# Optimization experiments

Hardware: AMD Instinct MI355X
Metric: run time of the kernel (lower is better)

## Reference

```python
import jax, jax.numpy as jnp
import numpy as np

B, C1, C2, N1, N2 = 8, 16, 32, 256, 128


def _masks():
    # static numpy masks, mirroring EquivariantLayer.__init__
    n_max, n_min = max(N1, N2), min(N1, N2)
    k = np.arange(n_max)
    k[k > n_max // 2] -= n_max
    mask = np.abs(k) <= n_min / 2            # |k| <= n_min/2 (both nyquists)
    mask2 = mask[: n_max // 2 + 1].copy()    # taken BEFORE removing neg nyquist
    nyq_pos = k == n_min / 2
    nyq_pos2 = nyq_pos[: n_max // 2 + 1]
    nyq_neg = k == -n_min / 2
    mask[nyq_neg] = False                    # drop negative nyquist row
    return mask, mask2, nyq_pos, nyq_pos2

MASK, MASK2, NYQ_POS, NYQ_POS2 = _masks()


def rot90_kernel(t):
    # 90-deg rotation about grid point [0,0] for periodic kernels:
    # transpose last two dims, keep column 0, reverse remaining columns
    t = jnp.swapaxes(t, -1, -2)
    return jnp.concatenate([t[..., :1], t[..., 1:][..., ::-1]], axis=-1)


def symmetric_kernel(kernel):
    # average over the 8 elements of D4 (rotations + transpose*rotations)
    k1 = kernel
    k2 = rot90_kernel(k1)
    k3 = rot90_kernel(k2)
    k4 = rot90_kernel(k3)
    k5 = jnp.swapaxes(k1, -1, -2)
    k6 = rot90_kernel(k5)
    k7 = rot90_kernel(k6)
    k8 = rot90_kernel(k7)
    return (k1 + k2 + k3 + k4 + k5 + k6 + k7 + k8) / 8.0


def _forward(f, kernel):
    F = jnp.fft.rfft2(f)                                  # [b,c1,N1,N1//2+1]
    # downsample: zero nyquist modes, truncate spectrum, rescale
    F = jnp.where(jnp.asarray(NYQ_POS)[None, None, :, None], 0, F)
    F = jnp.where(jnp.asarray(NYQ_POS2)[None, None, None, :], 0, F)
    F = F[:, :, MASK, :][:, :, :, MASK2] * (N2 / N1) ** 2  # [b,c1,N2,N2//2+1]
    # spectral convolution with D4-symmetrized kernel
    K = jnp.fft.rfft2(symmetric_kernel(kernel))            # [1,c1,c2,N2,N2//2+1]
    conv = jnp.einsum('bcnk,cdnk->bdnk', F, K[0])          # sum over input channels
    return jnp.fft.irfft2(F), jnp.fft.irfft2(conv)


def setup_inputs() -> dict:
    key = jax.random.key(0)
    kf, kk = jax.random.split(key)
    f = jax.random.normal(kf, (B, C1, N1, N1), dtype=jnp.float32)
    eps = 0.1
    kernel = eps * (2.0 * jax.random.uniform(kk, (1, C1, C2, N2, N2), dtype=jnp.float32) - 1.0)
    return {"f": f, "kernel": kernel}


def reference(f, kernel):
    return _forward(f, kernel)
```

## Files before the change

### kernel.cpp

```cpp
#include <hip/hip_runtime.h>

#define PI_F 3.14159265358979f

typedef unsigned int  uint32;
typedef unsigned short ushort16;

__device__ __forceinline__ float2 cmul(float2 a, float2 b) {
    return make_float2(a.x * b.x - a.y * b.y, a.x * b.y + a.y * b.x);
}
__device__ __forceinline__ float2 cadd(float2 a, float2 b) { return make_float2(a.x + b.x, a.y + b.y); }
__device__ __forceinline__ float2 csub(float2 a, float2 b) { return make_float2(a.x - b.x, a.y - b.y); }
__device__ __forceinline__ float2 shflx(float2 v, int m) {
    return make_float2(__shfl_xor(v.x, m, 64), __shfl_xor(v.y, m, 64));
}
__device__ __forceinline__ float2 shfli(float2 v, int src) {
    return make_float2(__shfl(v.x, src, 64), __shfl(v.y, src, 64));
}
__device__ __forceinline__ int brev6(int x) { return (int)(__brev((unsigned)x) >> 26); }

__device__ __forceinline__ uint32 bfu(float x) {
    uint32 u = __float_as_uint(x);
    return (u + 0x7FFFu + ((u >> 16) & 1u)) >> 16;
}
__device__ __forceinline__ uint32 packbf2(float2 v) { return bfu(v.x) | (bfu(v.y) << 16); }
__device__ __forceinline__ float2 unpackbf2(uint32 u) {
    return make_float2(__uint_as_float(u << 16), __uint_as_float(u & 0xFFFF0000u));
}
__device__ __forceinline__ float bf2f(ushort16 u) { return __uint_as_float((uint32)u << 16); }

template<int CTRL>
__device__ __forceinline__ float dpp1(float x) {
    return __builtin_bit_cast(float, __builtin_amdgcn_update_dpp(
        0, __builtin_bit_cast(int, x), CTRL, 0xF, 0xF, true));
}
template<int CTRL>
__device__ __forceinline__ float2 dppx(float2 v) {
    return make_float2(dpp1<CTRL>(v.x), dpp1<CTRL>(v.y));
}

__device__ __forceinline__ float swz4(float x) {
    return __int_as_float(__builtin_amdgcn_ds_swizzle(__float_as_int(x), 0x101F));
}

template<bool INV>
__device__ __forceinline__ void tw_init(int lane, float2* w, float* sg) {
#pragma unroll
    for (int t = 0; t < 6; ++t) {
        int m = 32 >> t;
        bool up = (lane & m) != 0;
        int pos = lane & (m - 1);
        float ang = (INV ? PI_F : -PI_F) * (float)pos / (float)m;
        float sn, cs;
        __sincosf(ang, &sn, &cs);
        w[t]  = up ? make_float2(cs, sn) : make_float2(1.f, 0.f);
        sg[t] = (t < 2) ? (up ? -2.f : 0.f) : (up ? -1.f : 1.f);
    }
}

__device__ __forceinline__ float2 fft64s(float2 v, const float2* w, const float* sg) {
#if __has_builtin(__builtin_amdgcn_permlane32_swap) && __has_builtin(__builtin_amdgcn_permlane16_swap)
    {
        auto rx = __builtin_amdgcn_permlane32_swap(__float_as_uint(v.x), __float_as_uint(v.x), false, false);
        auto ry = __builtin_amdgcn_permlane32_swap(__float_as_uint(v.y), __float_as_uint(v.y), false, false);
        float2 d = make_float2(
            fmaf(sg[0], v.x, __uint_as_float(rx[0]) + __uint_as_float(rx[1])),
            fmaf(sg[0], v.y, __uint_as_float(ry[0]) + __uint_as_float(ry[1])));
        v = cmul(d, w[0]);
    }
    {
        auto rx = __builtin_amdgcn_permlane16_swap(__float_as_uint(v.x), __float_as_uint(v.x), false, false);
        auto ry = __builtin_amdgcn_permlane16_swap(__float_as_uint(v.y), __float_as_uint(v.y), false, false);
        float2 d = make_float2(
            fmaf(sg[1], v.x, __uint_as_float(rx[0]) + __uint_as_float(rx[1])),
            fmaf(sg[1], v.y, __uint_as_float(ry[0]) + __uint_as_float(ry[1])));
        v = cmul(d, w[1]);
    }
#else
    {   float2 p = shflx(v, 32); float s0 = 1.0f + sg[0];
        float2 d = make_float2(fmaf(s0, v.x, p.x), fmaf(s0, v.y, p.y));
        v = cmul(d, w[0]);
    }
    {   float2 p = shflx(v, 16); float s1 = 1.0f + sg[1];
        float2 d = make_float2(fmaf(s1, v.x, p.x), fmaf(s1, v.y, p.y));
        v = cmul(d, w[1]);
    }
#endif
    {
        float2 p = dppx<0x128>(v);
        float2 d = make_float2(fmaf(sg[2], v.x, p.x), fmaf(sg[2], v.y, p.y));
        v = cmul(d, w[2]);
    }
    {
        float2 p = make_float2(swz4(v.x), swz4(v.y));
        float2 d = make_float2(fmaf(sg[3], v.x, p.x), fmaf(sg[3], v.y, p.y));
        v = cmul(d, w[3]);
    }
    {
        float2 p = dppx<0x4E>(v);
        float2 d = make_float2(fmaf(sg[4], v.x, p.x), fmaf(sg[4], v.y, p.y));
        v = cmul(d, w[4]);
    }
    {
        float2 p = dppx<0xB1>(v);
        float2 d = make_float2(fmaf(sg[5], v.x, p.x), fmaf(sg[5], v.y, p.y));
        v = cmul(d, w[5]);
    }
    return v;
}

__device__ __forceinline__ int s66(int r, int c) {
    return r * 66 + (c ^ (((r >> 4) & 3) << 4));
}

__device__ void kfft_body(const float* __restrict__ kin, ushort16* __restrict__ kout,
                          float2* X, int img) {
    int lane = threadIdx.x & 63, wv = threadIdx.x >> 6;
    float2 w[6]; float sg[6];
    tw_init<false>(lane, w, sg);
    int b6 = brev6(lane);
    float sn, cs;
    __sincosf(-PI_F * (float)lane * (1.0f / 64.0f), &sn, &cs);
    float2 w64 = make_float2(cs, sn);
    __sincosf(-PI_F * (float)b6 * (1.0f / 64.0f), &sn, &cs);
    float2 wub = make_float2(cs, sn);
    const float2* in2 = (const float2*)(kin + (size_t)img * 16384);
    int gm2 = brev6((64 - b6) & 63);
#pragma unroll 2
    for (int rr = 0; rr < 16; ++rr) {
        int r = wv * 16 + rr;
        float2 z = in2[r * 64 + lane];
        z = fft64s(z, w, sg);
        float2 zm = shfli(z, gm2);
        float ar = z.x + zm.x, ai = z.y - zm.y;
        float br = z.x - zm.x, bi = z.y + zm.y;
        float p = wub.x * br - wub.y * bi, q = wub.x * bi + wub.y * br;
        X[r * 65 + b6] = make_float2(0.5f * (ar + q), 0.5f * (ai - p));
    }
    __syncthreads();
    float2 c0[8], c1[8];
#pragma unroll
    for (int cc = 0; cc < 8; ++cc) {
        int k = wv * 8 + cc;
        c0[cc] = X[lane * 65 + k];
        c1[cc] = X[(lane + 64) * 65 + k];
    }
    __syncthreads();
    float* Rr = (float*)X;
#pragma unroll
    for (int cc = 0; cc < 8; ++cc) {
        int k = wv * 8 + cc;
        float2 r0 = c0[cc], r1 = c1[cc];
        float2 t = r0;
        r0 = cadd(t, r1);
        r1 = cmul(csub(t, r1), w64);
        r0 = fft64s(r0, w, sg);
        r1 = fft64s(r1, w, sg);
        Rr[(2 * b6) * 65 + k]     = r0.x;
        Rr[(2 * b6 + 1) * 65 + k] = r1.x;
    }
    __syncthreads();
    ushort4* ko4 = (ushort4*)(kout + (size_t)img * 8192);
    for (int i = threadIdx.x; i < 2048; i += 512) {
        int n = i >> 4, k4 = (i & 15) << 2;
        float op[4];
#pragma unroll
        for (int m = 0; m < 4; ++m) {
            int k = k4 + m;
            float t1 = Rr[n * 65 + k];
            float t2 = Rr[((128 - n) & 127) * 65 + k];
            float t3, t4;
            if (n < 64) {
                t3 = Rr[k * 65 + n];
                t4 = Rr[((128 - k) & 127) * 65 + n];
            } else {
                int c2 = 128 - n; if (c2 > 63) c2 = 63;
                t3 = Rr[((128 - k) & 127) * 65 + c2];
                t4 = Rr[k * 65 + c2];
            }
            op[m] = 0.25f * (t1 + t2 + t3 + t4);
        }
        ushort4 o4;
        o4.x = (ushort16)bfu(op[0]); o4.y = (ushort16)bfu(op[1]);
        o4.z = (ushort16)bfu(op[2]); o4.w = (ushort16)bfu(op[3]);
        ko4[i] = o4;
    }
}

__device__ void ffull_body(const float* __restrict__ f, uint32* __restrict__ FH,
                           uint32* S, int img) {
    int lane = threadIdx.x & 63, wv = threadIdx.x >> 6;
    float2 w[6]; float sg[6];
    tw_init<false>(lane, w, sg);
    float sn, cs;
    __sincosf(-PI_F * (float)lane * (1.0f / 64.0f), &sn, &cs);
    float2 w64 = make_float2(cs, sn);
    int m = brev6(lane);
    __sincosf(-PI_F * (float)(2 * m) * (1.0f / 128.0f), &sn, &cs);
    float2 wue = make_float2(cs, sn);
    __sincosf(-PI_F * (float)(2 * m + 1) * (1.0f / 128.0f), &sn, &cs);
    float2 wuo = make_float2(cs, sn);
    int src_e = brev6((64 - m) & 63);
    int src_o = brev6(63 - m);
    bool active = (lane & 1) == 0;
    const float* fimg = f + (size_t)img * 65536;
#pragma unroll 2
    for (int rr = 0; rr < 32; ++rr) {
        int r = wv * 32 + rr;
        const float2* x = (const float2*)(fimg + r * 256);
        float2 r0 = x[lane], r1 = x[lane + 64];
        float2 t = r0;
        r0 = cadd(t, r1);
        r1 = cmul(csub(t, r1), w64);
        r0 = fft64s(r0, w, sg);
        r1 = fft64s(r1, w, sg);
        float2 zme = shfli(r0, src_e);
        float2 zmo = shfli(r1, src_o);
        float ar = r0.x + zme.x, ai = r0.y - zme.y;
        float br = r0.x - zme.x, bi = r0.y + zme.y;
        float p = wue.x * br - wue.y * bi, q = wue.x * bi + wue.y * br;
        uint32 xe = packbf2(make_float2(0.5f * (ar + q), 0.5f * (ai - p)));
        ar = r1.x + zmo.x; ai = r1.y - zmo.y;
        br = r1.x - zmo.x; bi = r1.y + zmo.y;
        p = wuo.x * br - wuo.y * bi; q = wuo.x * bi + wuo.y * br;
        uint32 xo = packbf2(make_float2(0.5f * (ar + q), 0.5f * (ai - p)));
        if (active) *(uint2*)&S[s66(r, 2 * m)] = make_uint2(xe, xo);
    }
    __syncthreads();
    __sincosf(-PI_F * (float)lane * (1.0f / 128.0f), &sn, &cs);
    float2 w128a = make_float2(cs, sn);
    __sincosf(-PI_F * (float)(lane + 64) * (1.0f / 128.0f), &sn, &cs);
    float2 w128b = make_float2(cs, sn);
    int b6 = brev6(lane);
#pragma unroll
    for (int ch = 0; ch < 4; ++ch) {
        float2 q0[2], q1[2], q2[2], q3[2];
#pragma unroll
        for (int cc = 0; cc < 2; ++cc) {
            int c = wv * 8 + ch * 2 + cc;
            q0[cc] = unpackbf2(S[s66(lane,       c)]);
            q1[cc] = unpackbf2(S[s66(lane +  64, c)]);
            q2[cc] = unpackbf2(S[s66(lane + 128, c)]);
            q3[cc] = unpackbf2(S[s66(lane + 192, c)]);
        }
#pragma unroll
        for (int cc = 0; cc < 2; ++cc) {
            int c = wv * 8 + ch * 2 + cc;
            float2 r0 = q0[cc], r1 = q1[cc], r2 = q2[cc], r3 = q3[cc], t;
            t = r0; r0 = cadd(t, r2); r2 = cmul(csub(t, r2), w128a);
            t = r1; r1 = cadd(t, r3); r3 = cmul(csub(t, r3), w128b);
            t = r0; r0 = cadd(t, r1); r1 = cmul(csub(t, r1), w64);
            t = r2; r2 = cadd(t, r3); r3 = cmul(csub(t, r3), w64);
            r0 = fft64s(r0, w, sg); r1 = fft64s(r1, w, sg);
            r2 = fft64s(r2, w, sg); r3 = fft64s(r3, w, sg);
            float2 vv[4] = { r0, r2, r1, r3 };
#pragma unroll
            for (int j = 0; j < 4; ++j) {
                int n = 4 * b6 + j;
                int r = (n < 64) ? n : ((n >= 193) ? n - 128 : -1);
                if (r >= 0)
                    S[s66(r, c)] = packbf2(make_float2(vv[j].x * 0.25f, vv[j].y * 0.25f));
            }
        }
    }
    __syncthreads();
    uint32* dst = FH + (size_t)img * 8192;
    for (int i = threadIdx.x; i < 8192; i += 512) {
        int r = i >> 6, c = i & 63;
        dst[i] = (r == 64) ? 0u : S[s66(r, c)];
    }
}

__global__ __launch_bounds__(512) void mega_a(const float* __restrict__ kin,
                                              ushort16* __restrict__ Kr,
                                              const float* __restrict__ f,
                                              uint32* __restrict__ FH) {
    __shared__ uint32 SH[256 * 66];
    int bid = blockIdx.x;
    if (bid < 128) ffull_body(f, FH, SH, bid);
    else           kfft_body(kin, Kr, (float2*)SH, bid - 128);
}

__device__ void einsum_body(const uint32* __restrict__ F, const ushort16* __restrict__ K,
                            uint32* __restrict__ C, uint32* Ft, int bid) {
    int nk0 = bid * 32;
    int t = threadIdx.x;
    for (int i = t; i < 4096; i += 512) {
        int bc = i >> 5, nl = i & 31;
        Ft[i] = F[(size_t)bc * 8192 + nk0 + nl];
    }
    __syncthreads();
    int nl = t & 31, dg = t >> 5;
    int nk = nk0 + nl;
    float2 acc[2][8] = {};
#pragma unroll
    for (int c = 0; c < 16; ++c) {
        float2 fv[8];
#pragma unroll
        for (int b = 0; b < 8; ++b) fv[b] = unpackbf2(Ft[(b * 16 + c) * 32 + nl]);
#pragma unroll
        for (int j = 0; j < 2; ++j) {
            int d = j * 16 + dg;
            float kv = bf2f(K[(size_t)(c * 32 + d) * 8192 + nk]);
#pragma unroll
            for (int b = 0; b < 8; ++b) {
                acc[j][b].x = fmaf(fv[b].x, kv, acc[j][b].x);
                acc[j][b].y = fmaf(fv[b].y, kv, acc[j][b].y);
            }
        }
    }
#pragma unroll
    for (int j = 0; j < 2; ++j) {
        int d = j * 16 + dg;
#pragma unroll
        for (int b = 0; b < 8; ++b)
            C[(size_t)(b * 32 + d) * 8192 + nk] = packbf2(acc[j][b]);
    }
}

__device__ void ifuse_body(const uint32* __restrict__ src, float2* __restrict__ dst,
                           float2* S) {
    int lane = threadIdx.x & 63, wv = threadIdx.x >> 6;
    float2 w[6]; float sg[6];
    tw_init<true>(lane, w, sg);
    float sn, cs;
    __sincosf(PI_F * (float)lane * (1.0f / 64.0f), &sn, &cs);
    float2 w64 = make_float2(cs, sn);
    for (int i = threadIdx.x; i < 8192; i += 512) {
        int r = i >> 6, c = i & 63;
        S[r * 65 + c] = unpackbf2(src[i]);
    }
    __syncthreads();
    int b6 = brev6(lane);
#pragma unroll
    for (int cc = 0; cc < 8; ++cc) {
        int k = wv * 8 + cc;
        float2 r0 = S[lane * 65 + k];
        float2 r1 = S[(lane + 64) * 65 + k];
        float2 t = r0;
        r0 = cadd(t, r1);
        r1 = cmul(csub(t, r1), w64);
        r0 = fft64s(r0, w, sg);
        r1 = fft64s(r1, w, sg);
        S[(2 * b6) * 65 + k]     = r0;
        S[(2 * b6 + 1) * 65 + k] = r1;
    }
    __syncthreads();
#pragma unroll 2
    for (int rr = 0; rr < 16; ++rr) {
        int m = wv * 16 + rr;
        float2 X = S[m * 65 + lane];
        float2 Xm = shfli(X, (64 - lane) & 63);
        if (lane == 0) Xm = make_float2(0.f, 0.f);
        float er = 0.5f * (X.x + Xm.x), ei = 0.5f * (X.y - Xm.y);
        float br = 0.5f * (X.x - Xm.x), bi = 0.5f * (X.y + Xm.y);
        float orr = w64.x * br - w64.y * bi, oi = w64.x * bi + w64.y * br;
        float2 Z = make_float2(er - oi, ei + orr);
        Z = fft64s(Z, w, sg);
        dst[m * 64 + b6] = make_float2(Z.x * (1.0f / 8192.0f), Z.y * (1.0f / 8192.0f));
    }
}

__global__ __launch_bounds__(512) void mega2(const uint32* __restrict__ FH,
                                             const ushort16* __restrict__ Kr,
                                             uint32* __restrict__ CONV,
                                             float* __restrict__ out) {
    __shared__ float2 SH[128 * 65];
    int bid = blockIdx.x;
    if (bid < 256) einsum_body(FH, Kr, CONV, (uint32*)SH, bid);
    else {
        int img = bid - 256;
        ifuse_body(FH + (size_t)img * 8192, (float2*)(out + (size_t)img * 16384), SH);
    }
}

__global__ __launch_bounds__(512) void ifuse1(const uint32* __restrict__ CV,
                                              float* __restrict__ out1) {
    __shared__ float2 SH[128 * 65];
    int img = blockIdx.x;
    ifuse_body(CV + (size_t)img * 8192, (float2*)(out1 + (size_t)img * 16384), SH);
}

extern "C" void kernel_launch(void* const* d_in, const int* in_sizes, int n_in,
                              void* d_out, int out_size, void* d_ws, size_t ws_size,
                              hipStream_t stream) {
    const float* f   = (const float*)d_in[0];
    const float* kin = (const float*)d_in[1];
    float* out = (float*)d_out;
    char* ws = (char*)d_ws;

    uint32*   CONV = (uint32*)ws;
    uint32*   FHAT = (uint32*)(ws + 8388608);
    ushort16* Kr   = (ushort16*)(ws + 16777216);

    mega_a<<<640, 512, 0, stream>>>(kin, Kr, f, FHAT);
    mega2<<<384, 512, 0, stream>>>(FHAT, Kr, CONV, out);
    ifuse1<<<256, 512, 0, stream>>>(CONV, out + 2097152);
}
```

Before: 161.5 us.

## Fuse channel-contraction einsum into the inverse FFT blocks, dropping CONV buffer

Each inverse-FFT block for the conv output now computes its own (b,d) spectrum by contracting over the 16 input channels directly into shared memory, then runs the inverse FFT. This removes the separate einsum pass, the bf16 CONV round-trip through global memory, and one kernel launch. In exchange the F spectra are re-read once per output channel (32x redundancy, though likely L2-resident) and the K reads lose the batch reuse the old einsum had.

```diff
diff --git a/kernel.cpp b/kernel.cpp
--- a/kernel.cpp
+++ b/kernel.cpp
@@ -280,56 +280,13 @@
     else           kfft_body(kin, Kr, (float2*)SH, bid - 128);
 }
 
-__device__ void einsum_body(const uint32* __restrict__ F, const ushort16* __restrict__ K,
-                            uint32* __restrict__ C, uint32* Ft, int bid) {
-    int nk0 = bid * 32;
-    int t = threadIdx.x;
-    for (int i = t; i < 4096; i += 512) {
-        int bc = i >> 5, nl = i & 31;
-        Ft[i] = F[(size_t)bc * 8192 + nk0 + nl];
-    }
-    __syncthreads();
-    int nl = t & 31, dg = t >> 5;
-    int nk = nk0 + nl;
-    float2 acc[2][8] = {};
-#pragma unroll
-    for (int c = 0; c < 16; ++c) {
-        float2 fv[8];
-#pragma unroll
-        for (int b = 0; b < 8; ++b) fv[b] = unpackbf2(Ft[(b * 16 + c) * 32 + nl]);
-#pragma unroll
-        for (int j = 0; j < 2; ++j) {
-            int d = j * 16 + dg;
-            float kv = bf2f(K[(size_t)(c * 32 + d) * 8192 + nk]);
-#pragma unroll
-            for (int b = 0; b < 8; ++b) {
-                acc[j][b].x = fmaf(fv[b].x, kv, acc[j][b].x);
-                acc[j][b].y = fmaf(fv[b].y, kv, acc[j][b].y);
-            }
-        }
-    }
-#pragma unroll
-    for (int j = 0; j < 2; ++j) {
-        int d = j * 16 + dg;
-#pragma unroll
-        for (int b = 0; b < 8; ++b)
-            C[(size_t)(b * 32 + d) * 8192 + nk] = packbf2(acc[j][b]);
-    }
-}
-
-__device__ void ifuse_body(const uint32* __restrict__ src, float2* __restrict__ dst,
-                           float2* S) {
+__device__ void ifuse_core(float2* S, float2* __restrict__ dst) {
     int lane = threadIdx.x & 63, wv = threadIdx.x >> 6;
     float2 w[6]; float sg[6];
     tw_init<true>(lane, w, sg);
     float sn, cs;
     __sincosf(PI_F * (float)lane * (1.0f / 64.0f), &sn, &cs);
     float2 w64 = make_float2(cs, sn);
-    for (int i = threadIdx.x; i < 8192; i += 512) {
-        int r = i >> 6, c = i & 63;
-        S[r * 65 + c] = unpackbf2(src[i]);
-    }
-    __syncthreads();
     int b6 = brev6(lane);
 #pragma unroll
     for (int cc = 0; cc < 8; ++cc) {
@@ -360,24 +317,55 @@
     }
 }
 
-__global__ __launch_bounds__(512) void mega2(const uint32* __restrict__ FH,
-                                             const ushort16* __restrict__ Kr,
-                                             uint32* __restrict__ CONV,
-                                             float* __restrict__ out) {
+__device__ void ifuse_body(const uint32* __restrict__ src, float2* __restrict__ dst,
+                           float2* S) {
+    for (int i = threadIdx.x; i < 8192; i += 512) {
+        int r = i >> 6, c = i & 63;
+        S[r * 65 + c] = unpackbf2(src[i]);
+    }
+    __syncthreads();
+    ifuse_core(S, dst);
+}
+
+__device__ void convifuse_body(const uint32* __restrict__ FH,
+                               const uint32* __restrict__ Kr32,
+                               float2* __restrict__ dst, float2* S, int img) {
+    int b = img >> 5, d = img & 31;
+    int t = threadIdx.x;
+#pragma unroll 2
+    for (int p = 0; p < 8; ++p) {
+        int nk2 = (t + p * 512) * 2;
+        float2 a0 = make_float2(0.f, 0.f), a1 = make_float2(0.f, 0.f);
+#pragma unroll
+        for (int c = 0; c < 16; ++c) {
+            uint2  fv = *(const uint2*)&FH[((size_t)(b * 16 + c) << 13) + nk2];
+            uint32 kv = Kr32[((size_t)(c * 32 + d) << 12) + (nk2 >> 1)];
+            float2 kk = unpackbf2(kv);
+            float2 f0 = unpackbf2(fv.x), f1 = unpackbf2(fv.y);
+            a0.x = fmaf(f0.x, kk.x, a0.x); a0.y = fmaf(f0.y, kk.x, a0.y);
+            a1.x = fmaf(f1.x, kk.y, a1.x); a1.y = fmaf(f1.y, kk.y, a1.y);
+        }
+        int r = nk2 >> 6, cc = nk2 & 63;
+        S[r * 65 + cc]     = a0;
+        S[r * 65 + cc + 1] = a1;
+    }
+    __syncthreads();
+    ifuse_core(S, dst);
+}
+
+__global__ __launch_bounds__(512) void mega_b(const uint32* __restrict__ FH,
+                                              const uint32* __restrict__ Kr32,
+                                              float* __restrict__ out) {
     __shared__ float2 SH[128 * 65];
     int bid = blockIdx.x;
-    if (bid < 256) einsum_body(FH, Kr, CONV, (uint32*)SH, bid);
-    else {
+    if (bid < 256) {
+        int img = bid;
+        convifuse_body(FH, Kr32, (float2*)(out + 2097152 + (size_t)img * 16384),
+                       SH, img);
+    } else {
         int img = bid - 256;
         ifuse_body(FH + (size_t)img * 8192, (float2*)(out + (size_t)img * 16384), SH);
     }
-}
-
-__global__ __launch_bounds__(512) void ifuse1(const uint32* __restrict__ CV,
-                                              float* __restrict__ out1) {
-    __shared__ float2 SH[128 * 65];
-    int img = blockIdx.x;
-    ifuse_body(CV + (size_t)img * 8192, (float2*)(out1 + (size_t)img * 16384), SH);
 }
 
 extern "C" void kernel_launch(void* const* d_in, const int* in_sizes, int n_in,
@@ -388,11 +376,9 @@
     float* out = (float*)d_out;
     char* ws = (char*)d_ws;
 
-    uint32*   CONV = (uint32*)ws;
     uint32*   FHAT = (uint32*)(ws + 8388608);
     ushort16* Kr   = (ushort16*)(ws + 16777216);
 
     mega_a<<<640, 512, 0, stream>>>(kin, Kr, f, FHAT);
-    mega2<<<384, 512, 0, stream>>>(FHAT, Kr, CONV, out);
-    ifuse1<<<256, 512, 0, stream>>>(CONV, out + 2097152);
-}
+    mega_b<<<384, 512, 0, stream>>>(FHAT, (const uint32*)Kr, out);
+}
```

Measured after the change: 165.5 us. 1.02x slower.

## Split einsum into standalone kernel and batch all inverse FFTs together

Applied to the files above, without the earlier changes.

The einsum runs as its own kernel with a small static shared buffer, instead of sharing a launch with the inverse FFT of the downsampled input. Both inverse-FFT workloads (the conv output and F) are then merged into one 384-block kernel. The intent is to raise einsum occupancy by dropping the large shared allocation and to balance the final kernel's block mix. The cost is losing the overlap of F's inverse FFT with the einsum.

```diff
diff --git a/kernel.cpp b/kernel.cpp
--- a/kernel.cpp
+++ b/kernel.cpp
@@ -280,8 +280,11 @@
     else           kfft_body(kin, Kr, (float2*)SH, bid - 128);
 }
 
-__device__ void einsum_body(const uint32* __restrict__ F, const ushort16* __restrict__ K,
-                            uint32* __restrict__ C, uint32* Ft, int bid) {
+__global__ __launch_bounds__(512) void einsum_k(const uint32* __restrict__ F,
+                                                const ushort16* __restrict__ K,
+                                                uint32* __restrict__ C) {
+    __shared__ uint32 Ft[4096];
+    int bid = blockIdx.x;
     int nk0 = bid * 32;
     int t = threadIdx.x;
     for (int i = t; i < 4096; i += 512) {
@@ -360,24 +363,20 @@
     }
 }
 
-__global__ __launch_bounds__(512) void mega2(const uint32* __restrict__ FH,
-                                             const ushort16* __restrict__ Kr,
-                                             uint32* __restrict__ CONV,
-                                             float* __restrict__ out) {
+__global__ __launch_bounds__(512) void ifuse_all(const uint32* __restrict__ FH,
+                                                 const uint32* __restrict__ CV,
+                                                 float* __restrict__ out) {
     __shared__ float2 SH[128 * 65];
     int bid = blockIdx.x;
-    if (bid < 256) einsum_body(FH, Kr, CONV, (uint32*)SH, bid);
-    else {
+    if (bid < 256) {
+        int img = bid;
+        ifuse_body(CV + (size_t)img * 8192,
+                   (float2*)(out + 2097152 + (size_t)img * 16384), SH);
+    } else {
         int img = bid - 256;
-        ifuse_body(FH + (size_t)img * 8192, (float2*)(out + (size_t)img * 16384), SH);
-    }
-}
-
-__global__ __launch_bounds__(512) void ifuse1(const uint32* __restrict__ CV,
-                                              float* __restrict__ out1) {
-    __shared__ float2 SH[128 * 65];
-    int img = blockIdx.x;
-    ifuse_body(CV + (size_t)img * 8192, (float2*)(out1 + (size_t)img * 16384), SH);
+        ifuse_body(FH + (size_t)img * 8192,
+                   (float2*)(out + (size_t)img * 16384), SH);
+    }
 }
 
 extern "C" void kernel_launch(void* const* d_in, const int* in_sizes, int n_in,
@@ -393,6 +392,6 @@
     ushort16* Kr   = (ushort16*)(ws + 16777216);
 
     mega_a<<<640, 512, 0, stream>>>(kin, Kr, f, FHAT);
-    mega2<<<384, 512, 0, stream>>>(FHAT, Kr, CONV, out);
-    ifuse1<<<256, 512, 0, stream>>>(CONV, out + 2097152);
-}
+    einsum_k<<<256, 512, 0, stream>>>(FHAT, Kr, CONV);
+    ifuse_all<<<384, 512, 0, stream>>>(FHAT, CONV, out);
+}
```

Result: faster. 152.4 us (-5.7%).
